# Performance work log

Measured on AMD Instinct MI355X. Metric: run time of the kernel, lower is better.

Reference implementation:

```python
import jax, jax.numpy as jnp
import numpy as np

B, T, C, H = 2, 2048, 1024, 16
D = C // H  # head_dim = 64


def setup_inputs() -> dict:
    key = jax.random.key(0)
    ks = jax.random.split(key, 5)
    x = jax.random.normal(ks[0], (B, T, C), dtype=jnp.float32)
    # fused QKV projection: Linear(C, 3C)
    W_qkv = jax.random.normal(ks[1], (C, 3 * C), dtype=jnp.float32) / np.sqrt(C)
    b_qkv = jax.random.normal(ks[2], (3 * C,), dtype=jnp.float32) * 0.02
    # output projection: Linear(C, C)
    W_proj = jax.random.normal(ks[3], (C, C), dtype=jnp.float32) / np.sqrt(C)
    b_proj = jax.random.normal(ks[4], (C,), dtype=jnp.float32) * 0.02
    return {"x": x, "W_qkv": W_qkv, "b_qkv": b_qkv, "W_proj": W_proj, "b_proj": b_proj}


def reference(x, W_qkv, b_qkv, W_proj, b_proj):
    # fused QKV projection
    qkv = jnp.einsum("btc,cd->btd", x, W_qkv) + b_qkv  # [B,T,3C]
    q, k, v = jnp.split(qkv, 3, axis=-1)
    # [B,T,C] -> [B,H,T,D]
    def to_heads(t):
        return t.reshape(B, T, H, D).transpose(0, 2, 1, 3)
    q, k, v = to_heads(q), to_heads(k), to_heads(v)
    # causal scaled dot-product attention (SDPA default scale = 1/sqrt(head_dim))
    scale = 1.0 / np.sqrt(D).astype(np.float32)
    scores = jnp.einsum("bhqd,bhkd->bhqk", q, k) * scale  # [B,H,T,T]
    causal = jnp.tril(jnp.ones((T, T), dtype=bool))
    scores = jnp.where(causal, scores, jnp.finfo(scores.dtype).min)
    attn = jax.nn.softmax(scores, axis=-1)
    out = jnp.einsum("bhqk,bhkd->bhqd", attn, v)  # [B,H,T,D]
    out = out.transpose(0, 2, 1, 3).reshape(B, T, C)
    # output projection
    return jnp.einsum("btc,cd->btd", out, W_proj) + b_proj
```

## Files before the change

kernel.cpp:

```cpp
#include <hip/hip_runtime.h>
#include <hip/hip_bf16.h>

typedef __attribute__((ext_vector_type(8))) __bf16 bf16x8;
typedef __attribute__((ext_vector_type(8))) short short8;
typedef __attribute__((ext_vector_type(4))) float f32x4;
typedef __attribute__((ext_vector_type(16))) float f32x16;
typedef __attribute__((ext_vector_type(4))) short sh4;

typedef __attribute__((address_space(1))) void GVoid;
typedef __attribute__((address_space(3))) void LVoid;

#define NEGBIG (-1e30f)
#define SCL 0.18033688011112042f

constexpr int TT = 2048, CC = 1024, HH = 16, DD = 64, C3 = 3072;

__device__ __forceinline__ unsigned short f2bf(float f) {
  unsigned int i = __float_as_uint(f);
  return (unsigned short)((i + 0x7FFFu + ((i >> 16) & 1u)) >> 16);
}
__device__ __forceinline__ void async16(const void* g, void* l) {
  __builtin_amdgcn_global_load_lds((GVoid*)g, (LVoid*)l, 16, 0, 0);
}

__global__ __launch_bounds__(256) void cvt_bf16(
    const float* __restrict__ in, unsigned short* __restrict__ out, int n8)
{
  const int i = blockIdx.x * 256 + threadIdx.x;
  if (i >= n8) return;
  const float* p = in + (size_t)i * 8;
  f32x4 a = *(const f32x4*)p, b = *(const f32x4*)(p + 4);
  sh4 r0, r1;
  ((unsigned short*)&r0)[0] = f2bf(a[0]); ((unsigned short*)&r0)[1] = f2bf(a[1]);
  ((unsigned short*)&r0)[2] = f2bf(a[2]); ((unsigned short*)&r0)[3] = f2bf(a[3]);
  ((unsigned short*)&r1)[0] = f2bf(b[0]); ((unsigned short*)&r1)[1] = f2bf(b[1]);
  ((unsigned short*)&r1)[2] = f2bf(b[2]); ((unsigned short*)&r1)[3] = f2bf(b[3]);
  *(sh4*)(out + (size_t)i * 8) = r0;
  *(sh4*)(out + (size_t)i * 8 + 4) = r1;
}

__global__ __launch_bounds__(256) void transpose_cvt(
    const float* __restrict__ in, unsigned short* __restrict__ out, int R, int Cd)
{
  __shared__ __align__(16) unsigned short tile[64 * 72];
  const int r0 = blockIdx.y * 64, c0 = blockIdx.x * 64;
  const int tid = threadIdx.x;
#pragma unroll
  for (int r = 0; r < 2; ++r) {
    const int elem = r * 2048 + tid * 8;
    const int ii = elem >> 6, jj = elem & 63;
    const float* p = in + (size_t)(r0 + ii) * Cd + c0 + jj;
    f32x4 a = *(const f32x4*)p, b = *(const f32x4*)(p + 4);
    short8 v;
    ((unsigned short*)&v)[0] = f2bf(a[0]); ((unsigned short*)&v)[1] = f2bf(a[1]);
    ((unsigned short*)&v)[2] = f2bf(a[2]); ((unsigned short*)&v)[3] = f2bf(a[3]);
    ((unsigned short*)&v)[4] = f2bf(b[0]); ((unsigned short*)&v)[5] = f2bf(b[1]);
    ((unsigned short*)&v)[6] = f2bf(b[2]); ((unsigned short*)&v)[7] = f2bf(b[3]);
    *(short8*)&tile[ii * 72 + jj] = v;
  }
  __syncthreads();
#pragma unroll
  for (int r = 0; r < 2; ++r) {
    const int elem = r * 2048 + tid * 8;
    const int jj = elem >> 6, ii0 = elem & 63;
    short8 v;
#pragma unroll
    for (int e = 0; e < 8; ++e) ((unsigned short*)&v)[e] = tile[(ii0 + e) * 72 + jj];
    *(short8*)&out[(size_t)(c0 + jj) * R + r0 + ii0] = v;
  }
}

template <int MODE>
__global__ __launch_bounds__(256) void gemm_bt(
    const unsigned short* __restrict__ A,
    const unsigned short* __restrict__ Bt,
    const float* __restrict__ bias,
    void* __restrict__ Cp, unsigned short* __restrict__ Vt,
    int M, int N, int K, int lda)
{
  __shared__ __align__(16) unsigned short sA[128 * 32];
  __shared__ __align__(16) unsigned short sB[128 * 32];
  const int tid = threadIdx.x;
  const int w = tid >> 6, l = tid & 63, ln = l & 15, quad = l >> 4;
  const int wm = w >> 1, wn = w & 1;
  const int m0 = blockIdx.y * 128, n0 = blockIdx.x * 128;
  f32x4 acc[4][4] = {};

  for (int k0 = 0; k0 < K; k0 += 32) {
    __syncthreads();
#pragma unroll
    for (int r = 0; r < 2; ++r) {
      const int elem = r * 2048 + tid * 8;
      const int ar = elem >> 5, ac = elem & 31;
      async16(A  + (size_t)(m0 + ar) * lda + k0 + ac, sA + r * 2048 + w * 512);
      async16(Bt + (size_t)(n0 + ar) * K   + k0 + ac, sB + r * 2048 + w * 512);
    }
    __syncthreads();

    bf16x8 af[4], bfr[4];
#pragma unroll
    for (int i = 0; i < 4; i++)
      af[i] = *(const bf16x8*)&sA[(wm * 64 + i * 16 + ln) * 32 + quad * 8];
#pragma unroll
    for (int j = 0; j < 4; j++)
      bfr[j] = *(const bf16x8*)&sB[(wn * 64 + j * 16 + ln) * 32 + quad * 8];
#pragma unroll
    for (int i = 0; i < 4; i++)
#pragma unroll
      for (int j = 0; j < 4; j++)
        acc[i][j] = __builtin_amdgcn_mfma_f32_16x16x32_bf16(af[i], bfr[j], acc[i][j], 0, 0, 0);
  }

  float bj[4];
#pragma unroll
  for (int j = 0; j < 4; j++) bj[j] = bias[n0 + wn * 64 + j * 16 + ln];

#pragma unroll
  for (int i = 0; i < 4; i++) {
#pragma unroll
    for (int j = 0; j < 4; j++) {
      const int gn = n0 + wn * 64 + j * 16 + ln;
      if (MODE == 0 && gn >= 2048) {
        const int hh = (gn >> 6) & 15, dd = gn & 63;
        const int gm0 = m0 + wm * 64 + i * 16 + quad * 4;
        const int bb = gm0 >> 11, t0 = gm0 & 2047;
        sh4 rv;
#pragma unroll
        for (int g = 0; g < 4; ++g)
          ((unsigned short*)&rv)[g] = f2bf(acc[i][j][g] + bj[j]);
        *(sh4*)&Vt[((size_t)((bb * HH + hh) * DD + dd)) * TT + t0] = rv;
      } else {
#pragma unroll
        for (int g = 0; g < 4; ++g) {
          const int gm = m0 + wm * 64 + i * 16 + quad * 4 + g;
          float v = acc[i][j][g] + bj[j];
          if (MODE == 0) {
            if (gn < 1024) v *= SCL;
            ((unsigned short*)Cp)[(size_t)gm * 2048 + gn] = f2bf(v);
          } else {
            ((float*)Cp)[(size_t)gm * N + gn] = v;
          }
        }
      }
    }
  }
}

__global__ __launch_bounds__(256) void gemm_n64(
    const unsigned short* __restrict__ A,
    const unsigned short* __restrict__ Bt,
    const float* __restrict__ bias,
    float* __restrict__ Cp, int M, int N, int K, int lda)
{
  __shared__ __align__(16) unsigned short sA[128 * 32];
  __shared__ __align__(16) unsigned short sB[64 * 32];
  const int tid = threadIdx.x;
  const int w = tid >> 6, l = tid & 63, ln = l & 15, quad = l >> 4;
  const int wm = w >> 1, wn = w & 1;
  const int m0 = blockIdx.y * 128, n0 = blockIdx.x * 64;
  f32x4 acc[4][2] = {};

  for (int k0 = 0; k0 < K; k0 += 32) {
    __syncthreads();
#pragma unroll
    for (int r = 0; r < 2; ++r) {
      const int elem = r * 2048 + tid * 8;
      const int ar = elem >> 5, ac = elem & 31;
      async16(A + (size_t)(m0 + ar) * lda + k0 + ac, sA + r * 2048 + w * 512);
    }
    {
      const int elem = tid * 8;
      const int ar = elem >> 5, ac = elem & 31;
      async16(Bt + (size_t)(n0 + ar) * K + k0 + ac, sB + w * 512);
    }
    __syncthreads();

    bf16x8 af[4], bfr[2];
#pragma unroll
    for (int i = 0; i < 4; i++)
      af[i] = *(const bf16x8*)&sA[(wm * 64 + i * 16 + ln) * 32 + quad * 8];
#pragma unroll
    for (int j = 0; j < 2; j++)
      bfr[j] = *(const bf16x8*)&sB[(wn * 32 + j * 16 + ln) * 32 + quad * 8];
#pragma unroll
    for (int i = 0; i < 4; i++)
#pragma unroll
      for (int j = 0; j < 2; j++)
        acc[i][j] = __builtin_amdgcn_mfma_f32_16x16x32_bf16(af[i], bfr[j], acc[i][j], 0, 0, 0);
  }

  float bj[2];
#pragma unroll
  for (int j = 0; j < 2; j++) bj[j] = bias[n0 + wn * 32 + j * 16 + ln];

#pragma unroll
  for (int i = 0; i < 4; i++)
#pragma unroll
    for (int g = 0; g < 4; ++g) {
      const int gm = m0 + wm * 64 + i * 16 + quad * 4 + g;
#pragma unroll
      for (int j = 0; j < 2; j++) {
        const int gn = n0 + wn * 32 + j * 16 + ln;
        Cp[(size_t)gm * N + gn] = acc[i][j][g] + bj[j];
      }
    }
}

__global__ __launch_bounds__(256) void attn32q(
    unsigned short* __restrict__ QK, const unsigned short* __restrict__ Vt)
{
  __shared__ __align__(16) unsigned short kt[2][64 * 72];
  __shared__ __align__(16) unsigned short vt[3][64 * 72];
  const int pair = blockIdx.x, bh = blockIdx.y;
  const int b = bh >> 4, h = bh & 15;
  const int tid = threadIdx.x, w = tid >> 6, l = tid & 63;
  const int c = l & 31, h2 = l >> 5;
  unsigned short*       Qp = QK + (size_t)b * TT * 2048 + h * DD;
  const unsigned short* Kp = QK + (size_t)b * TT * 2048 + CC + h * DD;
  const unsigned short* Vh = Vt + (size_t)bh * DD * TT;
  const int si0 = tid >> 3, so = (tid & 7) * 8;

  for (int ph = 0; ph < 2; ++ph) {
    const int qt = ph ? 15 - pair : pair;
    const int qbase = qt * 128 + w * 32;
    const int qm = qbase + c - 4 * h2;
    bf16x8 qv[4];
#pragma unroll
    for (int ds = 0; ds < 4; ++ds)
      qv[ds] = *(const bf16x8*)&Qp[(size_t)(qbase + c) * 2048 + ds * 16 + h2 * 8];

    f32x16 oacc[2] = {};
    bf16x8 pA[4] = {};
    float lsum = 0.0f;
    const int kbmax = 2 * qt + 1;
    int vm1 = 2, v0 = 0, vp1 = 1;

    __syncthreads();
#pragma unroll
    for (int r = 0; r < 2; ++r) {
      const int si = si0 + 32 * r;
      *(short8*)&kt[0][si * 72 + so] = *(const short8*)&Kp[(size_t)si * 2048 + so];
      *(short8*)&vt[0][si * 72 + so] = *(const short8*)&Vh[(size_t)si * TT + so];
    }
    __syncthreads();

    for (int kb = 0; kb <= kbmax; ++kb) {
      const int ck = kb & 1;
      short8 pk[2], pv[2];
      if (kb < kbmax) {
#pragma unroll
        for (int r = 0; r < 2; ++r) {
          const int si = si0 + 32 * r;
          pk[r] = *(const short8*)&Kp[(size_t)((kb + 1) * 64 + si) * 2048 + so];
          pv[r] = *(const short8*)&Vh[(size_t)si * TT + (kb + 1) * 64 + so];
        }
      }
      const bool qk_act = (kb * 64 <= qbase + 31);
      f32x16 sacc[2];
      if (qk_act) {
#pragma unroll
        for (int kg = 0; kg < 2; ++kg) {
          f32x16 sa = {};
#pragma unroll
          for (int ds = 0; ds < 4; ++ds) {
            bf16x8 kf = *(const bf16x8*)&kt[ck][(kg * 32 + c) * 72 + ds * 16 + h2 * 8];
            sa = __builtin_amdgcn_mfma_f32_32x32x16_bf16(kf, qv[ds], sa, 0, 0, 0);
          }
          sacc[kg] = sa;
        }
      }
      if (kb > 0 && (kb - 1) * 64 <= qbase + 31) {
        const unsigned short* vp = vt[vm1];
#pragma unroll
        for (int dg = 0; dg < 2; ++dg)
#pragma unroll
          for (int ks = 0; ks < 4; ++ks) {
            bf16x8 vf = *(const bf16x8*)&vp[(dg * 32 + c) * 72 + ks * 16 + h2 * 8];
            oacc[dg] = __builtin_amdgcn_mfma_f32_32x32x16_bf16(pA[ks], vf, oacc[dg], 0, 0, 0);
          }
      }
      if (qk_act) {
        const bool need_mask = (kb * 64 + 63 > qbase);
        float pe[2][16];
#pragma unroll
        for (int kg = 0; kg < 2; ++kg)
#pragma unroll
          for (int rr = 0; rr < 16; ++rr) {
            float sv = sacc[kg][rr];
            if (need_mask) {
              const int krel = kb * 64 + kg * 32 + (rr & 3) + 8 * (rr >> 2);
              if (krel > qm) sv = NEGBIG;
            }
            const float e = exp2f(sv);
            pe[kg][rr] = e;
            lsum += e;
          }
        unsigned W0[2][4], W1[2][4];
#pragma unroll
        for (int kg = 0; kg < 2; ++kg)
#pragma unroll
          for (int r4 = 0; r4 < 4; ++r4) {
            asm("v_cvt_pk_bf16_f32 %0, %1, %2"
                : "=v"(W0[kg][r4]) : "v"(pe[kg][4 * r4 + 0]), "v"(pe[kg][4 * r4 + 1]));
            asm("v_cvt_pk_bf16_f32 %0, %1, %2"
                : "=v"(W1[kg][r4]) : "v"(pe[kg][4 * r4 + 2]), "v"(pe[kg][4 * r4 + 3]));
          }
#pragma unroll
        for (int ks = 0; ks < 4; ++ks) {
          const int kg = ks >> 1, sel = ks & 1;
          unsigned a0 = W0[kg][2 * sel], b0 = W0[kg][2 * sel + 1];
          unsigned a1 = W1[kg][2 * sel], b1 = W1[kg][2 * sel + 1];
          asm("v_permlane32_swap_b32 %0, %1" : "+v"(a0), "+v"(b0));
          asm("v_permlane32_swap_b32 %0, %1" : "+v"(a1), "+v"(b1));
          unsigned wds[4] = {a0, a1, b0, b1};
          pA[ks] = *(const bf16x8*)wds;
        }
      }
      if (kb < kbmax) {
#pragma unroll
        for (int r = 0; r < 2; ++r) {
          const int si = si0 + 32 * r;
          *(short8*)&kt[1 - ck][si * 72 + so] = pk[r];
          *(short8*)&vt[vp1][si * 72 + so] = pv[r];
        }
      }
      __syncthreads();
      const int t_ = vm1; vm1 = v0; v0 = vp1; vp1 = t_;
    }
    if (kbmax * 64 <= qbase + 31) {
      const unsigned short* vp = vt[vm1];
#pragma unroll
      for (int dg = 0; dg < 2; ++dg)
#pragma unroll
        for (int ks = 0; ks < 4; ++ks) {
          bf16x8 vf = *(const bf16x8*)&vp[(dg * 32 + c) * 72 + ks * 16 + h2 * 8];
          oacc[dg] = __builtin_amdgcn_mfma_f32_32x32x16_bf16(pA[ks], vf, oacc[dg], 0, 0, 0);
        }
    }
    lsum += __shfl_xor(lsum, 32);
    const float inv = 1.0f / lsum;
#pragma unroll
    for (int rr = 0; rr < 16; ++rr) {
      const int q_rel = (rr & 3) + 8 * (rr >> 2) + 4 * h2;
      const float iq = __shfl(inv, q_rel);
      const size_t trow = qbase + q_rel;
#pragma unroll
      for (int dg = 0; dg < 2; ++dg)
        Qp[trow * 2048 + dg * 32 + c] = f2bf(oacc[dg][rr] * iq);
    }
  }
}

extern "C" void kernel_launch(void* const* d_in, const int* in_sizes, int n_in,
                              void* d_out, int out_size, void* d_ws, size_t ws_size,
                              hipStream_t stream)
{
  (void)in_sizes; (void)n_in; (void)out_size; (void)ws_size;
  const float* x     = (const float*)d_in[0];
  const float* Wqkv  = (const float*)d_in[1];
  const float* bqkv  = (const float*)d_in[2];
  const float* Wproj = (const float*)d_in[3];
  const float* bproj = (const float*)d_in[4];

  unsigned short* QK     = (unsigned short*)d_ws;
  unsigned short* WqkvT  = QK + (size_t)4096 * 2048;
  unsigned short* WprojT = WqkvT;
  unsigned short* Vt = (unsigned short*)d_out;
  unsigned short* xb = Vt + (size_t)32 * 64 * 2048;

  cvt_bf16<<<dim3(4096 * 1024 / 8 / 256), 256, 0, stream>>>(x, xb, 4096 * 1024 / 8);
  transpose_cvt<<<dim3(C3 / 64, CC / 64), 256, 0, stream>>>(Wqkv, WqkvT, CC, C3);
  gemm_bt<0><<<dim3(C3 / 128, 4096 / 128), 256, 0, stream>>>(
      xb, WqkvT, bqkv, QK, Vt, 4096, C3, CC, CC);
  transpose_cvt<<<dim3(CC / 64, CC / 64), 256, 0, stream>>>(Wproj, WprojT, CC, CC);
  attn32q<<<dim3(8, 2 * HH), 256, 0, stream>>>(QK, Vt);
  gemm_n64<<<dim3(CC / 64, 4096 / 128), 256, 0, stream>>>(
      QK, WprojT, bproj, (float*)d_out, 4096, CC, CC, 2048);
}
```

Measured before the change: 217.8 us.

## Split attention KV range across two wave groups per block and merge partials

The attention kernel now launches 512 threads per block. Two groups of four waves each process alternating 64-key blocks for the same 128 query rows, then merge their partial outputs and row sums through shared memory before normalising. This doubles the waves working on each query tile, which should give more latency hiding, since the grid has only 256 blocks. The risk is higher LDS use (extra K/V buffers plus the merge scratch), which may limit occupancy, along with an extra barrier and the merge step. The exp2f call is also replaced with a raw v_exp_f32 instruction.

Result: faster. 185.7 us (-14.7%).

```diff
diff --git a/kernel.cpp b/kernel.cpp
--- a/kernel.cpp
+++ b/kernel.cpp
@@ -206,23 +206,27 @@
     }
 }
 
-__global__ __launch_bounds__(256) void attn32q(
+__global__ __launch_bounds__(512) void attn2g(
     unsigned short* __restrict__ QK, const unsigned short* __restrict__ Vt)
 {
-  __shared__ __align__(16) unsigned short kt[2][64 * 72];
-  __shared__ __align__(16) unsigned short vt[3][64 * 72];
+  __shared__ __align__(16) unsigned short kt[2][2][64 * 72];
+  __shared__ __align__(16) unsigned short vt[2][3][64 * 72];
+  __shared__ float Ox[4][2][16][64];
+  __shared__ float Lx[4][64];
   const int pair = blockIdx.x, bh = blockIdx.y;
   const int b = bh >> 4, h = bh & 15;
-  const int tid = threadIdx.x, w = tid >> 6, l = tid & 63;
+  const int tid = threadIdx.x;
+  const int grp = tid >> 8, gtid = tid & 255;
+  const int wg = (tid >> 6) & 3, l = tid & 63;
   const int c = l & 31, h2 = l >> 5;
   unsigned short*       Qp = QK + (size_t)b * TT * 2048 + h * DD;
   const unsigned short* Kp = QK + (size_t)b * TT * 2048 + CC + h * DD;
   const unsigned short* Vh = Vt + (size_t)bh * DD * TT;
-  const int si0 = tid >> 3, so = (tid & 7) * 8;
+  const int si0 = gtid >> 3, so = (gtid & 7) * 8;
 
   for (int ph = 0; ph < 2; ++ph) {
     const int qt = ph ? 15 - pair : pair;
-    const int qbase = qt * 128 + w * 32;
+    const int qbase = qt * 128 + wg * 32;
     const int qm = qbase + c - 4 * h2;
     bf16x8 qv[4];
 #pragma unroll
@@ -232,27 +236,31 @@
     f32x16 oacc[2] = {};
     bf16x8 pA[4] = {};
     float lsum = 0.0f;
-    const int kbmax = 2 * qt + 1;
+    const int nslot = qt + 1;
     int vm1 = 2, v0 = 0, vp1 = 1;
 
     __syncthreads();
 #pragma unroll
     for (int r = 0; r < 2; ++r) {
       const int si = si0 + 32 * r;
-      *(short8*)&kt[0][si * 72 + so] = *(const short8*)&Kp[(size_t)si * 2048 + so];
-      *(short8*)&vt[0][si * 72 + so] = *(const short8*)&Vh[(size_t)si * TT + so];
-    }
-    __syncthreads();
-
-    for (int kb = 0; kb <= kbmax; ++kb) {
-      const int ck = kb & 1;
+      *(short8*)&kt[grp][0][si * 72 + so] =
+          *(const short8*)&Kp[(size_t)(grp * 64 + si) * 2048 + so];
+      *(short8*)&vt[grp][0][si * 72 + so] =
+          *(const short8*)&Vh[(size_t)si * TT + grp * 64 + so];
+    }
+    __syncthreads();
+
+    for (int slot = 0; slot < nslot; ++slot) {
+      const int kb = 2 * slot + grp;
+      const int ck = slot & 1;
       short8 pk[2], pv[2];
-      if (kb < kbmax) {
+      if (slot + 1 < nslot) {
+        const int kbn = kb + 2;
 #pragma unroll
         for (int r = 0; r < 2; ++r) {
           const int si = si0 + 32 * r;
-          pk[r] = *(const short8*)&Kp[(size_t)((kb + 1) * 64 + si) * 2048 + so];
-          pv[r] = *(const short8*)&Vh[(size_t)si * TT + (kb + 1) * 64 + so];
+          pk[r] = *(const short8*)&Kp[(size_t)(kbn * 64 + si) * 2048 + so];
+          pv[r] = *(const short8*)&Vh[(size_t)si * TT + kbn * 64 + so];
         }
       }
       const bool qk_act = (kb * 64 <= qbase + 31);
@@ -263,14 +271,14 @@
           f32x16 sa = {};
 #pragma unroll
           for (int ds = 0; ds < 4; ++ds) {
-            bf16x8 kf = *(const bf16x8*)&kt[ck][(kg * 32 + c) * 72 + ds * 16 + h2 * 8];
+            bf16x8 kf = *(const bf16x8*)&kt[grp][ck][(kg * 32 + c) * 72 + ds * 16 + h2 * 8];
             sa = __builtin_amdgcn_mfma_f32_32x32x16_bf16(kf, qv[ds], sa, 0, 0, 0);
           }
           sacc[kg] = sa;
         }
       }
-      if (kb > 0 && (kb - 1) * 64 <= qbase + 31) {
-        const unsigned short* vp = vt[vm1];
+      if (slot > 0 && (kb - 2) * 64 <= qbase + 31) {
+        const unsigned short* vp = vt[grp][vm1];
 #pragma unroll
         for (int dg = 0; dg < 2; ++dg)
 #pragma unroll
@@ -291,7 +299,8 @@
               const int krel = kb * 64 + kg * 32 + (rr & 3) + 8 * (rr >> 2);
               if (krel > qm) sv = NEGBIG;
             }
-            const float e = exp2f(sv);
+            float e;
+            asm("v_exp_f32 %0, %1" : "=v"(e) : "v"(sv));
             pe[kg][rr] = e;
             lsum += e;
           }
@@ -316,19 +325,20 @@
           pA[ks] = *(const bf16x8*)wds;
         }
       }
-      if (kb < kbmax) {
+      if (slot + 1 < nslot) {
 #pragma unroll
         for (int r = 0; r < 2; ++r) {
           const int si = si0 + 32 * r;
-          *(short8*)&kt[1 - ck][si * 72 + so] = pk[r];
-          *(short8*)&vt[vp1][si * 72 + so] = pv[r];
+          *(short8*)&kt[grp][1 - ck][si * 72 + so] = pk[r];
+          *(short8*)&vt[grp][vp1][si * 72 + so] = pv[r];
         }
       }
       __syncthreads();
       const int t_ = vm1; vm1 = v0; v0 = vp1; vp1 = t_;
     }
-    if (kbmax * 64 <= qbase + 31) {
-      const unsigned short* vp = vt[vm1];
+    const int kb_last = 2 * qt + grp;
+    if (kb_last * 64 <= qbase + 31) {
+      const unsigned short* vp = vt[grp][vm1];
 #pragma unroll
       for (int dg = 0; dg < 2; ++dg)
 #pragma unroll
@@ -338,15 +348,29 @@
         }
     }
     lsum += __shfl_xor(lsum, 32);
-    const float inv = 1.0f / lsum;
-#pragma unroll
-    for (int rr = 0; rr < 16; ++rr) {
-      const int q_rel = (rr & 3) + 8 * (rr >> 2) + 4 * h2;
-      const float iq = __shfl(inv, q_rel);
-      const size_t trow = qbase + q_rel;
+    if (grp == 1) {
 #pragma unroll
       for (int dg = 0; dg < 2; ++dg)
-        Qp[trow * 2048 + dg * 32 + c] = f2bf(oacc[dg][rr] * iq);
+#pragma unroll
+        for (int rr = 0; rr < 16; ++rr) Ox[wg][dg][rr][l] = oacc[dg][rr];
+      Lx[wg][l] = lsum;
+    }
+    __syncthreads();
+    if (grp == 0) {
+      const float inv = 1.0f / (lsum + Lx[wg][l]);
+#pragma unroll
+      for (int dg = 0; dg < 2; ++dg)
+#pragma unroll
+        for (int rr = 0; rr < 16; ++rr) oacc[dg][rr] += Ox[wg][dg][rr][l];
+#pragma unroll
+      for (int rr = 0; rr < 16; ++rr) {
+        const int q_rel = (rr & 3) + 8 * (rr >> 2) + 4 * h2;
+        const float iq = __shfl(inv, q_rel);
+        const size_t trow = qbase + q_rel;
+#pragma unroll
+        for (int dg = 0; dg < 2; ++dg)
+          Qp[trow * 2048 + dg * 32 + c] = f2bf(oacc[dg][rr] * iq);
+      }
     }
   }
 }
@@ -373,7 +397,7 @@
   gemm_bt<0><<<dim3(C3 / 128, 4096 / 128), 256, 0, stream>>>(
       xb, WqkvT, bqkv, QK, Vt, 4096, C3, CC, CC);
   transpose_cvt<<<dim3(CC / 64, CC / 64), 256, 0, stream>>>(Wproj, WprojT, CC, CC);
-  attn32q<<<dim3(8, 2 * HH), 256, 0, stream>>>(QK, Vt);
+  attn2g<<<dim3(8, 2 * HH), 512, 0, stream>>>(QK, Vt);
   gemm_n64<<<dim3(CC / 64, 4096 / 128), 256, 0, stream>>>(
       QK, WprojT, bproj, (float*)d_out, 4096, CC, CC, 2048);
 }
```
